# Optimization experiments

Hardware: AMD Instinct MI355X
Metric: run time of the kernel (lower is better)

Reference implementation:

```python
import jax, jax.numpy as jnp
import numpy as np

# ctlib options layout: [views, dets, width, height, dImg, dDet, Ang0, dAng, s2r, d2r, binshift]
VIEWS = 512
DETS = 512
H_IMG = 256
W_IMG = 256
D_IMG = 0.006641
D_DET = 0.0072
ANG0 = 0.0
D_ANG = 2.0 * np.pi / VIEWS
S2R = 5.95
D2R = 4.906
VIRDET = D_DET * S2R / (S2R + D2R)  # virtual detector spacing at isocenter


def make_filter():
    # ramp (Ram-Lak) filter in spatial domain, length 2*dets-1
    x = np.arange(2 * DETS - 1) - DETS + 1
    x2 = np.where(x == 0, 1, x * x).astype(np.float64)
    f = np.where(np.abs(x) % 2 == 1, -1.0 / (np.pi ** 2 * x2 * VIRDET ** 2), 0.0)
    f = np.where(x == 0, 1.0 / (4.0 * VIRDET ** 2), f)
    return jnp.asarray(f, dtype=jnp.float32).reshape(1, 1, 1, -1)


def make_w():
    # cosine (distance) pre-weight * quadrature step (virdet * pi / views)
    u = (np.arange(DETS) - DETS / 2 + 0.5) * VIRDET
    w = S2R / np.sqrt(S2R ** 2 + u ** 2) * VIRDET * np.pi / VIEWS
    return jnp.asarray(w, dtype=jnp.float32).reshape(1, 1, 1, -1)


def setup_inputs() -> dict:
    key = jax.random.key(0)
    projection = jax.random.normal(key, (2, 1, VIEWS, DETS), dtype=jnp.float32)
    return {"projection": projection, "w": make_w(), "filt": make_filter()}


def ramp_filter(p, filt):
    # p: [B,1,V,D], filt: [1,1,1,2D-1] -> [B,1,V,D] (same padding along detector axis)
    return jax.lax.conv_general_dilated(
        p, filt, window_strides=(1, 1),
        padding=((0, 0), (DETS - 1, DETS - 1)),
        dimension_numbers=("NCHW", "OIHW", "NCHW"))


def backproject_sv(p):
    # pixel-driven equidistant fan-beam backprojection, one output channel per view
    # p: [B,1,V,D] -> [B,V,H,W]
    p3 = p[:, 0]  # [B,V,D]
    betas = ANG0 + D_ANG * jnp.arange(VIEWS, dtype=jnp.float32)
    cb = jnp.cos(betas)[:, None, None]  # [V,1,1]
    sb = jnp.sin(betas)[:, None, None]
    xs = ((jnp.arange(W_IMG, dtype=jnp.float32) - (W_IMG - 1) / 2.0) * D_IMG)[None, None, :]
    ys = (((H_IMG - 1) / 2.0 - jnp.arange(H_IMG, dtype=jnp.float32)) * D_IMG)[None, :, None]
    d = S2R - (xs * cb + ys * sb)               # [V,H,W] source-to-pixel depth
    u = S2R * (ys * cb - xs * sb) / d           # virtual-detector coordinate
    wgt = (S2R / d) ** 2                        # fan-beam U^{-2} weight
    t = u / VIRDET + (DETS - 1) / 2.0           # fractional detector index
    i0 = jnp.floor(t).astype(jnp.int32)
    frac = t - i0
    v0 = (i0 >= 0) & (i0 < DETS)
    v1 = (i0 + 1 >= 0) & (i0 + 1 < DETS)
    i0c = jnp.clip(i0, 0, DETS - 1)
    i1c = jnp.clip(i0 + 1, 0, DETS - 1)
    gather = jax.vmap(lambda pv, idx: pv[:, idx], in_axes=(1, 0), out_axes=1)
    vals0 = gather(p3, i0c)  # [B,V,H,W]
    vals1 = gather(p3, i1c)
    w0 = ((1.0 - frac) * v0)[None]
    w1 = (frac * v1)[None]
    return wgt[None] * (vals0 * w0 + vals1 * w1)


def reference(projection, w, filt):
    p = projection * w                 # per-detector ramp pre-weight
    p = ramp_filter(p, filt)           # full-width ramp convolution
    return backproject_sv(p)           # per-view backprojection [B,V,H,W]
```

## Files before the change

### kernel.cpp

```cpp
#include <hip/hip_runtime.h>
#include <math.h>

#define VIEWS 512
#define DETS  512

constexpr double S2R_D    = 5.95;
constexpr double D2R_D    = 4.906;
constexpr double DDET_D   = 0.0072;
constexpr double VIRDET_D = DDET_D * S2R_D / (S2R_D + D2R_D);
constexpr double DANG_D   = 2.0 * 3.14159265358979323846 / (double)VIEWS;

__global__ __launch_bounds__(256) void fbp_filter_kernel(
    const float* __restrict__ proj, const float* __restrict__ wq,
    const float* __restrict__ filt, float* __restrict__ wsf,
    float* __restrict__ trig)
{
    __shared__ __align__(16) float pwpad[2][1536];
    __shared__ __align__(16) float sfe[520];
    const int tid = threadIdx.x;
    const int bid = blockIdx.x;

    if (bid < 2) {
        int v = bid * 256 + tid;
        float beta = (float)DANG_D * (float)v;
        trig[v]         = cosf(beta);
        trig[VIEWS + v] = sinf(beta);
    }

    for (int i = tid; i < 520; i += 256)
        sfe[i] = (i < 512) ? filt[2 * i] : 0.0f;

    float4* pz = (float4*)&pwpad[0][0];
    #pragma unroll
    for (int i = 0; i < 3; ++i)
        pz[tid + 256 * i] = make_float4(0.f, 0.f, 0.f, 0.f);
    __syncthreads();

    {
        const int rl  = tid >> 7;
        const int t2  = tid & 127;
        const int row = bid * 2 + rl;
        const float4 p4 = *(const float4*)(proj + (size_t)row * DETS + 4 * t2);
        const float4 w4 = *(const float4*)(wq + 4 * t2);
        pwpad[rl][511 + 4 * t2 + 0] = p4.x * w4.x;
        pwpad[rl][511 + 4 * t2 + 1] = p4.y * w4.y;
        pwpad[rl][511 + 4 * t2 + 2] = p4.z * w4.z;
        pwpad[rl][511 + 4 * t2 + 3] = p4.w * w4.w;
    }
    __syncthreads();

    const int lane = tid & 63;
    const int warp = tid >> 6;
    const int rl2  = warp >> 1;
    const int wv   = warp & 1;
    const int d0   = 256 * wv + 4 * lane;
    const float* P = &pwpad[rl2][0];
    const int e_lo = wv ? 0 : 124;
    const int G    = wv ? 48 : 49;
    const float c0 = filt[511];

    float a0 = 0.f, a1 = 0.f, a2 = 0.f, a3 = 0.f;
    for (int g = 0; g < G; ++g) {
        const int e0 = e_lo + 8 * g;
        const float4 S0 = *(const float4*)&sfe[e0];
        const float4 S1 = *(const float4*)&sfe[e0 + 4];
        const float* Pb = P + d0 + 2 * e0;
        const float4 q0 = *(const float4*)(Pb + 0);
        const float4 q1 = *(const float4*)(Pb + 4);
        const float4 q2 = *(const float4*)(Pb + 8);
        const float4 q3 = *(const float4*)(Pb + 12);
        const float4 q4 = *(const float4*)(Pb + 16);
        const float p[20] = {q0.x,q0.y,q0.z,q0.w, q1.x,q1.y,q1.z,q1.w,
                             q2.x,q2.y,q2.z,q2.w, q3.x,q3.y,q3.z,q3.w,
                             q4.x,q4.y,q4.z,q4.w};
        const float s[8]  = {S0.x,S0.y,S0.z,S0.w, S1.x,S1.y,S1.z,S1.w};
        #pragma unroll
        for (int j = 0; j < 8; ++j) {
            a0 = fmaf(p[2*j + 0], s[j], a0);
            a1 = fmaf(p[2*j + 1], s[j], a1);
            a2 = fmaf(p[2*j + 2], s[j], a2);
            a3 = fmaf(p[2*j + 3], s[j], a3);
        }
    }
    a0 = fmaf(P[511 + d0 + 0], c0, a0);
    a1 = fmaf(P[511 + d0 + 1], c0, a1);
    a2 = fmaf(P[511 + d0 + 2], c0, a2);
    a3 = fmaf(P[511 + d0 + 3], c0, a3);

    const int row2 = bid * 2 + rl2;
    *(float4*)(wsf + (size_t)row2 * DETS + d0) = make_float4(a0, a1, a2, a3);
}

__global__ __launch_bounds__(256) void fbp_bp_kernel(
    const float* __restrict__ wsf, const float* __restrict__ trig,
    float* __restrict__ out)
{
    const int v = blockIdx.x >> 8;
    const int y = blockIdx.x & 255;
    const int x = threadIdx.x;
    const float cb = trig[v];
    const float sb = trig[VIEWS + v];
    const float xs = ((float)x - 127.5f) * 0.006641f;
    const float ys = (127.5f - (float)y) * 0.006641f;
    const float den = 5.95f - (xs * cb + ys * sb);
    float inv = __builtin_amdgcn_rcpf(den);
    inv = inv * (2.0f - den * inv);
    const float sw  = 5.95f * inv;
    const float wgt = sw * sw;
    const float u   = 5.95f * (ys * cb - xs * sb) * inv;
    const float t   = u * (float)(1.0 / VIRDET_D) + 255.5f;
    const float ft  = floorf(t);
    const int   i0  = (int)ft;
    const float fr  = t - ft;
    const float w0 = (i0 >= 0 && i0 < DETS)         ? (1.0f - fr) : 0.0f;
    const float w1 = (i0 + 1 >= 0 && i0 + 1 < DETS) ? fr          : 0.0f;
    const int i0c = min(max(i0, 0), DETS - 1);
    const int i1c = min(max(i0 + 1, 0), DETS - 1);
    const float* r0 = wsf + ((size_t)v << 9);
    const float* r1 = wsf + ((size_t)(VIEWS + v) << 9);
    const float o0 = wgt * (r0[i0c] * w0 + r0[i1c] * w1);
    const float o1 = wgt * (r1[i0c] * w0 + r1[i1c] * w1);
    const size_t pix = ((size_t)blockIdx.x << 8) + (size_t)x;
    __builtin_nontemporal_store(o0, out + pix);
    __builtin_nontemporal_store(o1, out + 33554432u + pix);
}

extern "C" void kernel_launch(void* const* d_in, const int* in_sizes, int n_in,
                              void* d_out, int out_size, void* d_ws, size_t ws_size,
                              hipStream_t stream) {
    const float* proj = (const float*)d_in[0];
    const float* wq   = (const float*)d_in[1];
    const float* filt = (const float*)d_in[2];
    float* out  = (float*)d_out;
    float* wsf  = (float*)d_ws;
    float* trig = wsf + (size_t)1024 * 512;

    hipLaunchKernelGGL(fbp_filter_kernel, dim3(512), dim3(256), 0, stream,
                       proj, wq, filt, wsf, trig);
    hipLaunchKernelGGL(fbp_bp_kernel, dim3(VIEWS * 256), dim3(256), 0, stream,
                       wsf, trig, out);
}
```

Baseline: 300.6 us.

## Stage view rows in LDS and compute 4 pixels per thread with vector stores

The backprojection kernel now covers 32 image rows per block and copies the two filtered detector rows for its view into shared memory once, so interpolation gathers read LDS instead of global memory. Each thread computes four adjacent pixels, reusing per-view trig products, and writes them with 16-byte nontemporal stores. The grid shrinks from 131072 to 4096 blocks. The aim is to cut gather traffic and store instruction count on a write-bound kernel, at the cost of fewer blocks in flight and more work per thread.

```diff
diff --git a/kernel.cpp b/kernel.cpp
--- a/kernel.cpp
+++ b/kernel.cpp
@@ -3,6 +3,8 @@
 
 #define VIEWS 512
 #define DETS  512
+
+typedef float f32x4 __attribute__((ext_vector_type(4)));
 
 constexpr double S2R_D    = 5.95;
 constexpr double D2R_D    = 4.906;
@@ -95,34 +97,59 @@
     const float* __restrict__ wsf, const float* __restrict__ trig,
     float* __restrict__ out)
 {
-    const int v = blockIdx.x >> 8;
-    const int y = blockIdx.x & 255;
-    const int x = threadIdx.x;
+    __shared__ __align__(16) float rows[2][DETS];
+    const int tid = threadIdx.x;
+    const int v  = blockIdx.x >> 3;
+    const int yc = blockIdx.x & 7;
+
+    {
+        const float* src = wsf + (((size_t)(tid >> 7) * VIEWS + v) << 9);
+        ((float4*)&rows[0][0])[tid] = ((const float4*)src)[tid & 127];
+    }
     const float cb = trig[v];
     const float sb = trig[VIEWS + v];
-    const float xs = ((float)x - 127.5f) * 0.006641f;
-    const float ys = (127.5f - (float)y) * 0.006641f;
-    const float den = 5.95f - (xs * cb + ys * sb);
-    float inv = __builtin_amdgcn_rcpf(den);
-    inv = inv * (2.0f - den * inv);
-    const float sw  = 5.95f * inv;
-    const float wgt = sw * sw;
-    const float u   = 5.95f * (ys * cb - xs * sb) * inv;
-    const float t   = u * (float)(1.0 / VIRDET_D) + 255.5f;
-    const float ft  = floorf(t);
-    const int   i0  = (int)ft;
-    const float fr  = t - ft;
-    const float w0 = (i0 >= 0 && i0 < DETS)         ? (1.0f - fr) : 0.0f;
-    const float w1 = (i0 + 1 >= 0 && i0 + 1 < DETS) ? fr          : 0.0f;
-    const int i0c = min(max(i0, 0), DETS - 1);
-    const int i1c = min(max(i0 + 1, 0), DETS - 1);
-    const float* r0 = wsf + ((size_t)v << 9);
-    const float* r1 = wsf + ((size_t)(VIEWS + v) << 9);
-    const float o0 = wgt * (r0[i0c] * w0 + r0[i1c] * w1);
-    const float o1 = wgt * (r1[i0c] * w0 + r1[i1c] * w1);
-    const size_t pix = ((size_t)blockIdx.x << 8) + (size_t)x;
-    __builtin_nontemporal_store(o0, out + pix);
-    __builtin_nontemporal_store(o1, out + 33554432u + pix);
+    __syncthreads();
+
+    const int xi = (tid & 63) * 4;
+    const int wv = tid >> 6;
+    const float xs0 = ((float)xi - 127.5f) * 0.006641f;
+    const float xc0 = xs0 * cb;
+    const float xs_sb0 = xs0 * sb;
+    const float dcb = 0.006641f * cb;
+    const float dsb = 0.006641f * sb;
+
+    #pragma unroll
+    for (int i = 0; i < 8; ++i) {
+        const int y = yc * 32 + i * 4 + wv;
+        const float ys = (127.5f - (float)y) * 0.006641f;
+        const float ysb = ys * sb;
+        const float ycb = ys * cb;
+        f32x4 o0, o1;
+        #pragma unroll
+        for (int j = 0; j < 4; ++j) {
+            const float xcb = xc0 + (float)j * dcb;
+            const float xsb = xs_sb0 + (float)j * dsb;
+            const float den = 5.95f - xcb - ysb;
+            float inv = __builtin_amdgcn_rcpf(den);
+            inv = inv * (2.0f - den * inv);
+            const float sw  = 5.95f * inv;
+            const float wgt = sw * sw;
+            const float u   = 5.95f * (ycb - xsb) * inv;
+            const float t   = u * (float)(1.0 / VIRDET_D) + 255.5f;
+            const float ft  = floorf(t);
+            const int   i0  = (int)ft;
+            const float fr  = t - ft;
+            const float w0 = (i0 >= 0 && i0 < DETS)         ? (1.0f - fr) : 0.0f;
+            const float w1 = (i0 + 1 >= 0 && i0 + 1 < DETS) ? fr          : 0.0f;
+            const int i0c = min(max(i0, 0), DETS - 1);
+            const int i1c = min(max(i0 + 1, 0), DETS - 1);
+            o0[j] = wgt * (rows[0][i0c] * w0 + rows[0][i1c] * w1);
+            o1[j] = wgt * (rows[1][i0c] * w0 + rows[1][i1c] * w1);
+        }
+        const size_t pix = (((size_t)v << 16) + ((size_t)y << 8) + (size_t)xi) >> 2;
+        __builtin_nontemporal_store(o0, (f32x4*)out + pix);
+        __builtin_nontemporal_store(o1, (f32x4*)out + 8388608u + pix);
+    }
 }
 
 extern "C" void kernel_launch(void* const* d_in, const int* in_sizes, int n_in,
@@ -137,6 +164,6 @@
 
     hipLaunchKernelGGL(fbp_filter_kernel, dim3(512), dim3(256), 0, stream,
                        proj, wq, filt, wsf, trig);
-    hipLaunchKernelGGL(fbp_bp_kernel, dim3(VIEWS * 256), dim3(256), 0, stream,
+    hipLaunchKernelGGL(fbp_bp_kernel, dim3(VIEWS * 8), dim3(256), 0, stream,
                        wsf, trig, out);
 }
```

Measured after the change: 287.9 us. -4.2%, faster.
